# Kernel tuning notes

Hardware: AMD Instinct MI355X
Metric: run time of the kernel (lower is better)

The kernel has to match this reference:

```python
import jax, jax.numpy as jnp
import numpy as np

DIM = 1024          # config.dim
HID = 1024          # config.expert_hidden, already multiple of 64
N_EXP = 8           # num_routed_experts
TOP_K = 2           # top_k_experts
N_LOOPS = 4         # recursive_loops
B, S = 4, 1024


def setup_inputs() -> dict:
    key = jax.random.key(0)
    ks = jax.random.split(key, 10)
    def init(k, shape, fan_in):
        return jax.random.normal(k, shape, jnp.float32) * (fan_in ** -0.5)
    return {
        "x": jax.random.normal(ks[0], (B, S, DIM), jnp.float32),
        # shared expert (stored as [in, out] so forward is x @ W)
        "sg": init(ks[1], (DIM, HID), DIM),
        "su": init(ks[2], (DIM, HID), DIM),
        "sd": init(ks[3], (HID, DIM), HID),
        # routed experts stacked: [E, in, out]
        "Wg": init(ks[4], (N_EXP, DIM, HID), DIM),
        "Wu": init(ks[5], (N_EXP, DIM, HID), DIM),
        "Wd": init(ks[6], (N_EXP, HID, DIM), HID),
        # router: Linear(2*dim -> E, bias=False), stored [2*dim, E]
        "Wr": init(ks[7], (2 * DIM, N_EXP), 2 * DIM),
        # loop embedding table [num_loops, dim]
        "loop_table": jax.random.normal(ks[8], (N_LOOPS, DIM), jnp.float32),
        "loop_idx": 1,
    }


def _swiglu(x, wg, wu, wd):
    return (jax.nn.silu(x @ wg) * (x @ wu)) @ wd


def reference(x, sg, su, sd, Wg, Wu, Wd, Wr, loop_table, loop_idx):
    b, s, d = x.shape
    n = b * s
    xf = x.reshape(n, d)

    # shared expert (always active)
    shared = _swiglu(xf, sg, su, sd)  # [n, d]

    # loop-aware router: concat(x, loop_emb) @ Wr
    loop_emb = loop_table[loop_idx]                               # [d]
    router_in = jnp.concatenate(
        [xf, jnp.broadcast_to(loop_emb, (n, d))], axis=-1)        # [n, 2d]
    logits = router_in @ Wr                                       # [n, E]
    probs = jax.nn.sigmoid(logits)
    topw, topi = jax.lax.top_k(probs, TOP_K)                      # [n, k]

    # combine weights: combine[n, e] = sum_k topw[n,k] * (topi[n,k]==e)
    combine = jnp.zeros((n, N_EXP), x.dtype).at[
        jnp.arange(n)[:, None], topi].add(topw)                   # [n, E]

    # per-expert SwiGLU, combined with routing weights.
    # (dense-over-experts formulation; math identical to sort/dispatch/scatter)
    gate = jnp.einsum('nd,edh->neh', xf, Wg)                      # [n, E, H]
    up = jnp.einsum('nd,edh->neh', xf, Wu)                        # [n, E, H]
    h = jax.nn.silu(gate) * up                                    # [n, E, H]
    routed = jnp.einsum('neh,ehd,ne->nd', h, Wd, combine)         # [n, d]

    return (shared + routed).reshape(b, s, d)
```

## Files before the change

### kernel.cpp

```cpp
#include <hip/hip_runtime.h>
#include <cstdint>
#include <cstddef>

typedef __attribute__((ext_vector_type(8))) short short8;
typedef __attribute__((ext_vector_type(4))) float floatx4;

#define NTOK   4096
#define NSLOT  12288
#define SHSLOT 8192
#define MAT_ELEMS (1024 * 1024)

__device__ __forceinline__ unsigned short f2b(float f) {
  unsigned u = __float_as_uint(f);
  u = (u + 0x7fffu + ((u >> 16) & 1u)) >> 16;
  return (unsigned short)u;
}
__device__ __forceinline__ float b2f(unsigned short b) {
  return __uint_as_float((unsigned)b << 16);
}

#define GLD16(gsrc, ldst)                                                              \
  __builtin_amdgcn_global_load_lds(                                                    \
      (const __attribute__((address_space(1))) unsigned int*)(gsrc),                   \
      (__attribute__((address_space(3))) unsigned int*)(ldst), 16, 0, 0)

#define T2PITCH 260

__global__ __launch_bounds__(256) void prep_kernel(
    const float* __restrict__ x, const float* __restrict__ Wr,
    const float* __restrict__ loopTable, const int* __restrict__ loopIdx,
    const float* __restrict__ Wg, const float* __restrict__ Wu,
    const float* __restrict__ Wd, const float* __restrict__ sg,
    const float* __restrict__ su, const float* __restrict__ sd,
    unsigned short* __restrict__ Xb, int* __restrict__ cnt,
    int* __restrict__ permSparse, float* __restrict__ wSparse,
    int2* __restrict__ tokenEPos, unsigned short* __restrict__ Wt) {
  __shared__ __align__(16) char shraw[128 * T2PITCH];
  float (*red)[16][8] = (float(*)[16][8])shraw;
  float (*sbias)[8] = (float(*)[8])(shraw + 2048);
  int* lcnt = (int*)(shraw + 2048 + 128);
  int* lbase = (int*)(shraw + 2048 + 160);

  int tid = threadIdx.x;
  int bid = blockIdx.x;

  if (bid >= 256) {
    int tt = bid - 256;
    int m = tt >> 6;
    int tl = tt & 63;
    int k0 = (tl >> 3) << 7;
    int n0 = (tl & 7) << 7;
    int type = m / 9, e = m % 9;
    const float* src;
    if (type == 0)      src = (e < 8) ? Wg + (size_t)e * MAT_ELEMS : sg;
    else if (type == 1) src = (e < 8) ? Wu + (size_t)e * MAT_ELEMS : su;
    else                src = (e < 8) ? Wd + (size_t)e * MAT_ELEMS : sd;

    int rsub = tid >> 5;
    int nl4 = (tid & 31) << 2;
    const float* srcb = src + (size_t)k0 * 1024 + n0;
#pragma unroll
    for (int j = 0; j < 16; ++j) {
      int r = (j << 3) + rsub;
      float4 v = *(const float4*)(srcb + (size_t)r * 1024 + nl4);
      char* p0 = shraw + (size_t)(nl4 + 0) * T2PITCH + (r << 1);
      *(unsigned short*)(p0)               = f2b(v.x);
      *(unsigned short*)(p0 + T2PITCH)     = f2b(v.y);
      *(unsigned short*)(p0 + 2 * T2PITCH) = f2b(v.z);
      *(unsigned short*)(p0 + 3 * T2PITCH) = f2b(v.w);
    }
    __syncthreads();

    int nrow = tid >> 4;
    int l16 = tid & 15;
    unsigned short* dstm = Wt + (size_t)m * MAT_ELEMS;
#pragma unroll
    for (int p = 0; p < 8; ++p) {
      int n = (p << 4) + nrow;
      const char* rb = shraw + (size_t)n * T2PITCH + (l16 << 4);
      uint4 o;
      o.x = *(const unsigned*)(rb + 0);
      o.y = *(const unsigned*)(rb + 4);
      o.z = *(const unsigned*)(rb + 8);
      o.w = *(const unsigned*)(rb + 12);
      *(uint4*)&dstm[(size_t)(n0 + n) * 1024 + k0 + (l16 << 3)] = o;
    }
    return;
  }

  int lane = tid & 63;
  int seg = __builtin_amdgcn_readfirstlane(tid >> 6);
  int tok0 = bid << 4;
  int t16 = lane >> 2;
  int part = lane & 3;
  int tok = tok0 + t16;

  if (tid < 8) lcnt[tid] = 0;

  float bp[8] = {0, 0, 0, 0, 0, 0, 0, 0};
  {
    const float* emb = loopTable + (size_t)(*loopIdx) * 1024;
    int d = seg * 256 + lane * 4;
    float4 ev = *(const float4*)(emb + d);
    float es[4] = {ev.x, ev.y, ev.z, ev.w};
#pragma unroll
    for (int r = 0; r < 4; r++) {
      const float4* w4 = (const float4*)(Wr + (size_t)(1024 + d + r) * 8);
      float4 wa = w4[0], wb = w4[1];
      float e1 = es[r];
      bp[0] += e1 * wa.x; bp[1] += e1 * wa.y; bp[2] += e1 * wa.z; bp[3] += e1 * wa.w;
      bp[4] += e1 * wb.x; bp[5] += e1 * wb.y; bp[6] += e1 * wb.z; bp[7] += e1 * wb.w;
    }
  }
#pragma unroll
  for (int off = 32; off > 0; off >>= 1)
#pragma unroll
    for (int e = 0; e < 8; e++) bp[e] += __shfl_xor(bp[e], off, 64);
  if (lane == 0)
#pragma unroll
    for (int e = 0; e < 8; e++) sbias[seg][e] = bp[e];

  float lg[8] = {0, 0, 0, 0, 0, 0, 0, 0};
  const float* xr = x + (size_t)tok * 1024 + seg * 256 + part * 64;
  const float* wrb = Wr + (size_t)(seg * 256 + part * 64) * 8;
  for (int i = 0; i < 64; i += 4) {
    float4 xv = *(const float4*)(xr + i);
    float xs[4] = {xv.x, xv.y, xv.z, xv.w};
#pragma unroll
    for (int r = 0; r < 4; r++) {
      const float4* w4 = (const float4*)(wrb + (size_t)(i + r) * 8);
      float4 wa = w4[0], wb = w4[1];
      float xv1 = xs[r];
      lg[0] += xv1 * wa.x; lg[1] += xv1 * wa.y; lg[2] += xv1 * wa.z; lg[3] += xv1 * wa.w;
      lg[4] += xv1 * wb.x; lg[5] += xv1 * wb.y; lg[6] += xv1 * wb.z; lg[7] += xv1 * wb.w;
    }
  }
#pragma unroll
  for (int off = 1; off < 4; off <<= 1)
#pragma unroll
    for (int e = 0; e < 8; e++) lg[e] += __shfl_xor(lg[e], off, 64);
  if (part == 0)
#pragma unroll
    for (int e = 0; e < 8; e++) red[seg][t16][e] = lg[e];
  __syncthreads();

  int i0s = 0, i1s = 0, pos0s = 0, pos1s = 0;
  float p0s = 0.f, p1s = 0.f;
  if (tid < 16) {
    float l[8];
#pragma unroll
    for (int e = 0; e < 8; e++)
      l[e] = red[0][tid][e] + red[1][tid][e] + red[2][tid][e] + red[3][tid][e] +
             sbias[0][e] + sbias[1][e] + sbias[2][e] + sbias[3][e];
    int i0 = 0; float l0 = l[0];
#pragma unroll
    for (int e = 1; e < 8; e++) if (l[e] > l0) { l0 = l[e]; i0 = e; }
    int i1 = -1; float l1 = -1e30f;
#pragma unroll
    for (int e = 0; e < 8; e++) if (e != i0 && l[e] > l1) { l1 = l[e]; i1 = e; }
    i0s = i0; i1s = i1;
    p0s = 1.0f / (1.0f + __expf(-l0));
    p1s = 1.0f / (1.0f + __expf(-l1));
    pos0s = atomicAdd(&lcnt[i0], 1);
    pos1s = atomicAdd(&lcnt[i1], 1);
  }
  __syncthreads();
  if (tid < 8) lbase[tid] = atomicAdd(&cnt[tid], lcnt[tid]);
  __syncthreads();
  if (tid < 16) {
    int tk = tok0 + tid;
    int pos0 = lbase[i0s] + pos0s;
    int pos1 = lbase[i1s] + pos1s;
    permSparse[i0s * NTOK + pos0] = tk; wSparse[i0s * NTOK + pos0] = p0s;
    permSparse[i1s * NTOK + pos1] = tk; wSparse[i1s * NTOK + pos1] = p1s;
    tokenEPos[tk * 2 + 0] = make_int2(i0s, pos0);
    tokenEPos[tk * 2 + 1] = make_int2(i1s, pos1);
  }

  const float4* xs4 = (const float4*)(x + (size_t)tok0 * 1024);
  uint2* dst = (uint2*)(Xb + (size_t)tok0 * 1024);
  for (int i = tid; i < 16 * 256; i += 256) {
    float4 v = xs4[i];
    uint2 pk;
    pk.x = (unsigned)f2b(v.x) | ((unsigned)f2b(v.y) << 16);
    pk.y = (unsigned)f2b(v.z) | ((unsigned)f2b(v.w) << 16);
    dst[i] = pk;
  }
}

__device__ __forceinline__ void expert_range(const int* __restrict__ cnt, int e,
                                             int& c, int& off) {
  if (e == 8) { c = NTOK; off = SHSLOT; return; }
  off = 0; c = 0;
#pragma unroll
  for (int i = 0; i < 8; i++) {
    int cv = cnt[i];
    if (i < e) off += cv;
    if (i == e) c = cv;
  }
}

__global__ __launch_bounds__(256, 2) void gateup_gemm(
    const unsigned short* __restrict__ Xb, const unsigned short* __restrict__ Wt,
    const int* __restrict__ cnt, const int* __restrict__ permSparse,
    const float* __restrict__ wSparse, unsigned short* __restrict__ Hbuf) {
  int e = blockIdx.z;
  int c, off;
  expert_range(cnt, e, c, off);
  int m0 = blockIdx.y << 7;
  if (m0 >= c) return;
  int row_base = off + m0;
  int valid_m = c - m0; if (valid_m > 128) valid_m = 128;
  int n0 = blockIdx.x << 7;

  __shared__ unsigned short sA[128 * 64];
  __shared__ unsigned short sG[128 * 64];
  __shared__ unsigned short sU[128 * 64];

  int tid = threadIdx.x;
  int wv = tid >> 6, lane = tid & 63;
  int wm = wv >> 1, wn = wv & 1;

  const unsigned short* Gg = Wt + (size_t)e * MAT_ELEMS + (size_t)n0 * 1024;
  const unsigned short* Ug = Wt + (size_t)(9 + e) * MAT_ELEMS + (size_t)n0 * 1024;

  int srow = lane >> 3, schunk = lane & 7;
  int swc = (schunk ^ srow) << 3;

  int myTok[4];
#pragma unroll
  for (int j = 0; j < 4; j++) {
    int r = m0 + (wv << 5) + (j << 3) + srow;
    if (e < 8) myTok[j] = (r < c) ? permSparse[e * NTOK + r] : 0;
    else       myTok[j] = (r < c) ? r : 0;
  }

  floatx4 accG[4][4], accU[4][4];
#pragma unroll
  for (int i = 0; i < 4; i++)
#pragma unroll
    for (int j = 0; j < 4; j++) {
      accG[i][j] = floatx4{0.f, 0.f, 0.f, 0.f};
      accU[i][j] = floatx4{0.f, 0.f, 0.f, 0.f};
    }

  for (int kk = 0; kk < 1024; kk += 64) {
    __syncthreads();
#pragma unroll
    for (int j = 0; j < 4; j++) {
      int rb = (wv << 5) + (j << 3);
      size_t gw = (size_t)(rb + srow) * 1024 + kk + swc;
      GLD16(Xb + (size_t)myTok[j] * 1024 + kk + swc, &sA[rb * 64]);
      GLD16(Gg + gw, &sG[rb * 64]);
      GLD16(Ug + gw, &sU[rb * 64]);
    }
    __syncthreads();
#pragma unroll
    for (int k0 = 0; k0 < 64; k0 += 32) {
      int swoff = (((lane >> 4) + (k0 >> 3)) ^ (lane & 7)) << 3;
      int arow = (wm << 6) + (lane & 15);
      short8 af[4];
#pragma unroll
      for (int mi = 0; mi < 4; mi++)
        af[mi] = *(const short8*)&sA[(arow + (mi << 4)) * 64 + swoff];
      int brow = (wn << 6) + (lane & 15);
#pragma unroll
      for (int ni = 0; ni < 4; ni++) {
        short8 gf = *(const short8*)&sG[(brow + (ni << 4)) * 64 + swoff];
        short8 uf = *(const short8*)&sU[(brow + (ni << 4)) * 64 + swoff];
#pragma unroll
        for (int mi = 0; mi < 4; mi++) {
          accG[mi][ni] = __builtin_amdgcn_mfma_f32_16x16x32_bf16(af[mi], gf, accG[mi][ni], 0, 0, 0);
          accU[mi][ni] = __builtin_amdgcn_mfma_f32_16x16x32_bf16(af[mi], uf, accU[mi][ni], 0, 0, 0);
        }
      }
    }
  }

  int colLane = lane & 15, quad = lane >> 4;
#pragma unroll
  for (int mi = 0; mi < 4; mi++) {
#pragma unroll
    for (int reg = 0; reg < 4; reg++) {
      int mrow = (wm << 6) + (mi << 4) + (quad << 2) + reg;
      if (mrow < valid_m) {
        int r = m0 + mrow;
        float w = (e < 8) ? wSparse[e * NTOK + r] : 1.0f;
        unsigned short* hr = Hbuf + (size_t)(row_base + mrow) * 1024 + n0 + (wn << 6) + colLane;
#pragma unroll
        for (int ni = 0; ni < 4; ni++) {
          float g = accG[mi][ni][reg];
          float u = accU[mi][ni][reg];
          float h = (g / (1.0f + __expf(-g))) * u * w;
          hr[ni << 4] = f2b(h);
        }
      }
    }
  }
}

__global__ __launch_bounds__(256, 2) void down_gemm(
    const unsigned short* __restrict__ Hbuf, const unsigned short* __restrict__ Wt,
    const int* __restrict__ cnt, unsigned short* __restrict__ Dbuf) {
  int e = blockIdx.z;
  int c, off;
  expert_range(cnt, e, c, off);
  int m0 = blockIdx.y << 7;
  if (m0 >= c) return;
  int row_base = off + m0;
  int valid_m = c - m0; if (valid_m > 128) valid_m = 128;
  int n0 = blockIdx.x << 7;

  __shared__ unsigned short sA[128 * 64];
  __shared__ unsigned short sB[128 * 64];

  int tid = threadIdx.x;
  int wv = tid >> 6, lane = tid & 63;
  int wm = wv >> 1, wn = wv & 1;

  const unsigned short* Ag = Hbuf + (size_t)row_base * 1024;
  const unsigned short* Bg = Wt + (size_t)(18 + e) * MAT_ELEMS + (size_t)n0 * 1024;

  int srow = lane >> 3, schunk = lane & 7;
  int swc = (schunk ^ srow) << 3;

  floatx4 acc[4][4];
#pragma unroll
  for (int i = 0; i < 4; i++)
#pragma unroll
    for (int j = 0; j < 4; j++) acc[i][j] = floatx4{0.f, 0.f, 0.f, 0.f};

  for (int kk = 0; kk < 1024; kk += 64) {
    __syncthreads();
#pragma unroll
    for (int j = 0; j < 4; j++) {
      int rb = (wv << 5) + (j << 3);
      size_t gw = (size_t)(rb + srow) * 1024 + kk + swc;
      GLD16(Ag + gw, &sA[rb * 64]);
      GLD16(Bg + gw, &sB[rb * 64]);
    }
    __syncthreads();
#pragma unroll
    for (int k0 = 0; k0 < 64; k0 += 32) {
      int swoff = (((lane >> 4) + (k0 >> 3)) ^ (lane & 7)) << 3;
      int arow = (wm << 6) + (lane & 15);
      short8 af[4];
#pragma unroll
      for (int mi = 0; mi < 4; mi++)
        af[mi] = *(const short8*)&sA[(arow + (mi << 4)) * 64 + swoff];
      int brow = (wn << 6) + (lane & 15);
#pragma unroll
      for (int ni = 0; ni < 4; ni++) {
        short8 bf = *(const short8*)&sB[(brow + (ni << 4)) * 64 + swoff];
#pragma unroll
        for (int mi = 0; mi < 4; mi++)
          acc[mi][ni] = __builtin_amdgcn_mfma_f32_16x16x32_bf16(af[mi], bf, acc[mi][ni], 0, 0, 0);
      }
    }
  }

  int colLane = lane & 15, quad = lane >> 4;
#pragma unroll
  for (int mi = 0; mi < 4; mi++) {
#pragma unroll
    for (int reg = 0; reg < 4; reg++) {
      int mrow = (wm << 6) + (mi << 4) + (quad << 2) + reg;
      if (mrow < valid_m) {
        unsigned short* dr = Dbuf + (size_t)(row_base + mrow) * 1024 + n0 + (wn << 6) + colLane;
#pragma unroll
        for (int ni = 0; ni < 4; ni++)
          dr[ni << 4] = f2b(acc[mi][ni][reg]);
      }
    }
  }
}

__global__ __launch_bounds__(256) void combine_kernel(
    const unsigned short* __restrict__ Dbuf, const int* __restrict__ cnt,
    const int2* __restrict__ tokenEPos, float* __restrict__ out) {
  __shared__ int soffs[8];
  if (threadIdx.x == 0) {
    int s = 0;
    for (int i = 0; i < 8; i++) { soffs[i] = s; s += cnt[i]; }
  }
  __syncthreads();
  int tok = (blockIdx.x << 1) + (threadIdx.x >> 7);
  int lane = threadIdx.x & 127;
  int2 a = tokenEPos[tok * 2 + 0];
  int2 b = tokenEPos[tok * 2 + 1];
  int s0 = soffs[a.x] + a.y;
  int s1 = soffs[b.x] + b.y;
  int ssh = SHSLOT + tok;
  int d = lane << 3;
  uint4 r0 = *(const uint4*)(Dbuf + (size_t)ssh * 1024 + d);
  uint4 r1 = *(const uint4*)(Dbuf + (size_t)s0 * 1024 + d);
  uint4 r2 = *(const uint4*)(Dbuf + (size_t)s1 * 1024 + d);
  float o[8];
  const unsigned* u0 = (const unsigned*)&r0;
  const unsigned* u1 = (const unsigned*)&r1;
  const unsigned* u2 = (const unsigned*)&r2;
#pragma unroll
  for (int i = 0; i < 4; i++) {
    o[2 * i + 0] = b2f((unsigned short)(u0[i] & 0xffff)) +
                   b2f((unsigned short)(u1[i] & 0xffff)) +
                   b2f((unsigned short)(u2[i] & 0xffff));
    o[2 * i + 1] = b2f((unsigned short)(u0[i] >> 16)) +
                   b2f((unsigned short)(u1[i] >> 16)) +
                   b2f((unsigned short)(u2[i] >> 16));
  }
  float* orow = out + (size_t)tok * 1024 + d;
  *(float4*)(orow + 0) = make_float4(o[0], o[1], o[2], o[3]);
  *(float4*)(orow + 4) = make_float4(o[4], o[5], o[6], o[7]);
}

extern "C" void kernel_launch(void* const* d_in, const int* in_sizes, int n_in,
                              void* d_out, int out_size, void* d_ws, size_t ws_size,
                              hipStream_t stream) {
  const float* x  = (const float*)d_in[0];
  const float* sg = (const float*)d_in[1];
  const float* su = (const float*)d_in[2];
  const float* sd = (const float*)d_in[3];
  const float* Wg = (const float*)d_in[4];
  const float* Wu = (const float*)d_in[5];
  const float* Wd = (const float*)d_in[6];
  const float* Wr = (const float*)d_in[7];
  const float* loopTable = (const float*)d_in[8];
  const int*   loopIdx   = (const int*)d_in[9];
  float* out = (float*)d_out;

  char* w = (char*)d_ws;
  unsigned short* Wt = (unsigned short*)w;    w += (size_t)27 * MAT_ELEMS * 2;
  unsigned short* Xb = (unsigned short*)w;    w += (size_t)NTOK * 1024 * 2;
  unsigned short* Hbuf = (unsigned short*)w;  w += (size_t)NSLOT * 1024 * 2;
  unsigned short* Dbuf = (unsigned short*)w;  w += (size_t)NSLOT * 1024 * 2;
  int*   cnt        = (int*)w;   w += 16 * 4;
  int*   permSparse = (int*)w;   w += (size_t)8 * NTOK * 4;
  float* wSparse    = (float*)w; w += (size_t)8 * NTOK * 4;
  int2*  tokenEPos  = (int2*)w;  w += (size_t)NTOK * 2 * 8;

  hipMemsetAsync(cnt, 0, 32, stream);
  prep_kernel<<<256 + 27 * 64, 256, 0, stream>>>(
      x, Wr, loopTable, loopIdx, Wg, Wu, Wd, sg, su, sd,
      Xb, cnt, permSparse, wSparse, tokenEPos, Wt);
  gateup_gemm<<<dim3(8, 32, 9), 256, 0, stream>>>(Xb, Wt, cnt, permSparse,
                                                  wSparse, Hbuf);
  down_gemm<<<dim3(8, 32, 9), 256, 0, stream>>>(Hbuf, Wt, cnt, Dbuf);
  combine_kernel<<<2048, 256, 0, stream>>>(Dbuf, cnt, tokenEPos, out);
}
```

Before: 294.3 us.

## Triple-buffer LDS k-tiles with async global-to-LDS loads in expert GEMMs

Replaces the single-buffered 64-wide k-loop in the gate/up and down GEMMs with a three-stage ring of 32-wide k-tiles. Loads for tile h+2 are issued before computing tile h, with explicit vmcnt waits and raw barriers, so global-to-LDS transfers overlap the MFMA work. The LDS layout is re-swizzled for the 32-wide tiles, and s_setprio raises wave priority around the MFMA block. LDS use grows, to 72KB per block for gate/up, which may limit the two-blocks-per-CU occupancy target, and the hand-counted vmcnt values must match the exact number of loads issued.

Result: slower. 304.9 us (+3.6%).

```diff
diff --git a/kernel.cpp b/kernel.cpp
--- a/kernel.cpp
+++ b/kernel.cpp
@@ -23,6 +23,8 @@
   __builtin_amdgcn_global_load_lds(                                                    \
       (const __attribute__((address_space(1))) unsigned int*)(gsrc),                   \
       (__attribute__((address_space(3))) unsigned int*)(ldst), 16, 0, 0)
+
+#define WAITVM(N) asm volatile("s_waitcnt vmcnt(" #N ")" ::: "memory")
 
 #define T2PITCH 260
 
@@ -213,9 +215,7 @@
   int valid_m = c - m0; if (valid_m > 128) valid_m = 128;
   int n0 = blockIdx.x << 7;
 
-  __shared__ unsigned short sA[128 * 64];
-  __shared__ unsigned short sG[128 * 64];
-  __shared__ unsigned short sU[128 * 64];
+  __shared__ __align__(16) char lds[3 * 24576];
 
   int tid = threadIdx.x;
   int wv = tid >> 6, lane = tid & 63;
@@ -224,15 +224,32 @@
   const unsigned short* Gg = Wt + (size_t)e * MAT_ELEMS + (size_t)n0 * 1024;
   const unsigned short* Ug = Wt + (size_t)(9 + e) * MAT_ELEMS + (size_t)n0 * 1024;
 
-  int srow = lane >> 3, schunk = lane & 7;
-  int swc = (schunk ^ srow) << 3;
-
-  int myTok[4];
-#pragma unroll
-  for (int j = 0; j < 4; j++) {
-    int r = m0 + (wv << 5) + (j << 3) + srow;
-    if (e < 8) myTok[j] = (r < c) ? permSparse[e * NTOK + r] : 0;
-    else       myTok[j] = (r < c) ? r : 0;
+  int g = lane >> 3, s8 = lane & 7, v = s8 ^ g;
+  int vr = v >> 2;
+  int c8 = (v & 3) << 3;
+  int rl[2]; rl[0] = (wv << 5) + (g << 1) + vr; rl[1] = rl[0] + 16;
+
+  const unsigned short* gA[2];
+#pragma unroll
+  for (int i = 0; i < 2; ++i) {
+    int r = m0 + rl[i];
+    int tok;
+    if (e < 8) tok = (r < c) ? permSparse[e * NTOK + r] : 0;
+    else       tok = (r < c) ? r : 0;
+    gA[i] = Xb + (size_t)tok * 1024;
+  }
+  const unsigned short* gG[2] = { Gg + (size_t)rl[0] * 1024, Gg + (size_t)rl[1] * 1024 };
+  const unsigned short* gU[2] = { Ug + (size_t)rl[0] * 1024, Ug + (size_t)rl[1] * 1024 };
+  int ib[2] = { (wv << 11), (wv << 11) + 1024 };
+
+  int q = lane >> 4;
+  int offA[4], offB[4];
+#pragma unroll
+  for (int i = 0; i < 4; ++i) {
+    int rA = (wm << 6) + (lane & 15) + (i << 4);
+    offA[i] = ((rA >> 1) << 7) + (((((rA & 1) << 2) + q) ^ ((rA >> 1) & 7)) << 4);
+    int rB = (wn << 6) + (lane & 15) + (i << 4);
+    offB[i] = ((rB >> 1) << 7) + (((((rB & 1) << 2) + q) ^ ((rB >> 1) & 7)) << 4);
   }
 
   floatx4 accG[4][4], accU[4][4];
@@ -244,38 +261,46 @@
       accU[i][j] = floatx4{0.f, 0.f, 0.f, 0.f};
     }
 
-  for (int kk = 0; kk < 1024; kk += 64) {
-    __syncthreads();
-#pragma unroll
-    for (int j = 0; j < 4; j++) {
-      int rb = (wv << 5) + (j << 3);
-      size_t gw = (size_t)(rb + srow) * 1024 + kk + swc;
-      GLD16(Xb + (size_t)myTok[j] * 1024 + kk + swc, &sA[rb * 64]);
-      GLD16(Gg + gw, &sG[rb * 64]);
-      GLD16(Ug + gw, &sU[rb * 64]);
-    }
-    __syncthreads();
-#pragma unroll
-    for (int k0 = 0; k0 < 64; k0 += 32) {
-      int swoff = (((lane >> 4) + (k0 >> 3)) ^ (lane & 7)) << 3;
-      int arow = (wm << 6) + (lane & 15);
-      short8 af[4];
-#pragma unroll
-      for (int mi = 0; mi < 4; mi++)
-        af[mi] = *(const short8*)&sA[(arow + (mi << 4)) * 64 + swoff];
-      int brow = (wn << 6) + (lane & 15);
-#pragma unroll
-      for (int ni = 0; ni < 4; ni++) {
-        short8 gf = *(const short8*)&sG[(brow + (ni << 4)) * 64 + swoff];
-        short8 uf = *(const short8*)&sU[(brow + (ni << 4)) * 64 + swoff];
-#pragma unroll
-        for (int mi = 0; mi < 4; mi++) {
-          accG[mi][ni] = __builtin_amdgcn_mfma_f32_16x16x32_bf16(af[mi], gf, accG[mi][ni], 0, 0, 0);
-          accU[mi][ni] = __builtin_amdgcn_mfma_f32_16x16x32_bf16(af[mi], uf, accU[mi][ni], 0, 0, 0);
-        }
+#define GU_STAGE(SB, H) do { int ke = ((H) << 5) + c8;                     \
+    GLD16(gA[0] + ke, lds + (SB) + ib[0]);                                 \
+    GLD16(gA[1] + ke, lds + (SB) + ib[1]);                                 \
+    GLD16(gG[0] + ke, lds + (SB) + 8192 + ib[0]);                          \
+    GLD16(gG[1] + ke, lds + (SB) + 8192 + ib[1]);                          \
+    GLD16(gU[0] + ke, lds + (SB) + 16384 + ib[0]);                         \
+    GLD16(gU[1] + ke, lds + (SB) + 16384 + ib[1]); } while (0)
+
+  int sb0 = 0, sb1 = 24576, sb2 = 49152;
+  GU_STAGE(sb0, 0);
+  GU_STAGE(sb1, 1);
+
+  for (int h = 0; h < 32; ++h) {
+    __builtin_amdgcn_s_barrier();
+    __builtin_amdgcn_sched_barrier(0);
+    if (h < 30) GU_STAGE(sb2, h + 2);
+    if (h < 30)       WAITVM(12);
+    else if (h == 30) WAITVM(6);
+    else              WAITVM(0);
+    __builtin_amdgcn_s_barrier();
+    __builtin_amdgcn_sched_barrier(0);
+    short8 af[4];
+#pragma unroll
+    for (int mi = 0; mi < 4; ++mi)
+      af[mi] = *(const short8*)(lds + sb0 + offA[mi]);
+    __builtin_amdgcn_s_setprio(1);
+#pragma unroll
+    for (int ni = 0; ni < 4; ++ni) {
+      short8 gf = *(const short8*)(lds + sb0 + 8192 + offB[ni]);
+      short8 uf = *(const short8*)(lds + sb0 + 16384 + offB[ni]);
+#pragma unroll
+      for (int mi = 0; mi < 4; ++mi) {
+        accG[mi][ni] = __builtin_amdgcn_mfma_f32_16x16x32_bf16(af[mi], gf, accG[mi][ni], 0, 0, 0);
+        accU[mi][ni] = __builtin_amdgcn_mfma_f32_16x16x32_bf16(af[mi], uf, accU[mi][ni], 0, 0, 0);
       }
     }
-  }
+    __builtin_amdgcn_s_setprio(0);
+    int t = sb0; sb0 = sb1; sb1 = sb2; sb2 = t;
+  }
+#undef GU_STAGE
 
   int colLane = lane & 15, quad = lane >> 4;
 #pragma unroll
@@ -289,10 +314,10 @@
         unsigned short* hr = Hbuf + (size_t)(row_base + mrow) * 1024 + n0 + (wn << 6) + colLane;
 #pragma unroll
         for (int ni = 0; ni < 4; ni++) {
-          float g = accG[mi][ni][reg];
+          float gg2 = accG[mi][ni][reg];
           float u = accU[mi][ni][reg];
-          float h = (g / (1.0f + __expf(-g))) * u * w;
-          hr[ni << 4] = f2b(h);
+          float hh = (gg2 / (1.0f + __expf(-gg2))) * u * w;
+          hr[ni << 4] = f2b(hh);
         }
       }
     }
@@ -311,8 +336,7 @@
   int valid_m = c - m0; if (valid_m > 128) valid_m = 128;
   int n0 = blockIdx.x << 7;
 
-  __shared__ unsigned short sA[128 * 64];
-  __shared__ unsigned short sB[128 * 64];
+  __shared__ __align__(16) char lds[3 * 16384];
 
   int tid = threadIdx.x;
   int wv = tid >> 6, lane = tid & 63;
@@ -321,8 +345,24 @@
   const unsigned short* Ag = Hbuf + (size_t)row_base * 1024;
   const unsigned short* Bg = Wt + (size_t)(18 + e) * MAT_ELEMS + (size_t)n0 * 1024;
 
-  int srow = lane >> 3, schunk = lane & 7;
-  int swc = (schunk ^ srow) << 3;
+  int g = lane >> 3, s8 = lane & 7, v = s8 ^ g;
+  int vr = v >> 2;
+  int c8 = (v & 3) << 3;
+  int rl[2]; rl[0] = (wv << 5) + (g << 1) + vr; rl[1] = rl[0] + 16;
+
+  const unsigned short* gA[2] = { Ag + (size_t)rl[0] * 1024, Ag + (size_t)rl[1] * 1024 };
+  const unsigned short* gB[2] = { Bg + (size_t)rl[0] * 1024, Bg + (size_t)rl[1] * 1024 };
+  int ib[2] = { (wv << 11), (wv << 11) + 1024 };
+
+  int q = lane >> 4;
+  int offA[4], offB[4];
+#pragma unroll
+  for (int i = 0; i < 4; ++i) {
+    int rA = (wm << 6) + (lane & 15) + (i << 4);
+    offA[i] = ((rA >> 1) << 7) + (((((rA & 1) << 2) + q) ^ ((rA >> 1) & 7)) << 4);
+    int rB = (wn << 6) + (lane & 15) + (i << 4);
+    offB[i] = ((rB >> 1) << 7) + (((((rB & 1) << 2) + q) ^ ((rB >> 1) & 7)) << 4);
+  }
 
   floatx4 acc[4][4];
 #pragma unroll
@@ -330,34 +370,41 @@
 #pragma unroll
     for (int j = 0; j < 4; j++) acc[i][j] = floatx4{0.f, 0.f, 0.f, 0.f};
 
-  for (int kk = 0; kk < 1024; kk += 64) {
-    __syncthreads();
-#pragma unroll
-    for (int j = 0; j < 4; j++) {
-      int rb = (wv << 5) + (j << 3);
-      size_t gw = (size_t)(rb + srow) * 1024 + kk + swc;
-      GLD16(Ag + gw, &sA[rb * 64]);
-      GLD16(Bg + gw, &sB[rb * 64]);
-    }
-    __syncthreads();
-#pragma unroll
-    for (int k0 = 0; k0 < 64; k0 += 32) {
-      int swoff = (((lane >> 4) + (k0 >> 3)) ^ (lane & 7)) << 3;
-      int arow = (wm << 6) + (lane & 15);
-      short8 af[4];
-#pragma unroll
-      for (int mi = 0; mi < 4; mi++)
-        af[mi] = *(const short8*)&sA[(arow + (mi << 4)) * 64 + swoff];
-      int brow = (wn << 6) + (lane & 15);
-#pragma unroll
-      for (int ni = 0; ni < 4; ni++) {
-        short8 bf = *(const short8*)&sB[(brow + (ni << 4)) * 64 + swoff];
-#pragma unroll
-        for (int mi = 0; mi < 4; mi++)
-          acc[mi][ni] = __builtin_amdgcn_mfma_f32_16x16x32_bf16(af[mi], bf, acc[mi][ni], 0, 0, 0);
-      }
-    }
-  }
+#define DN_STAGE(SB, H) do { int ke = ((H) << 5) + c8;                     \
+    GLD16(gA[0] + ke, lds + (SB) + ib[0]);                                 \
+    GLD16(gA[1] + ke, lds + (SB) + ib[1]);                                 \
+    GLD16(gB[0] + ke, lds + (SB) + 8192 + ib[0]);                          \
+    GLD16(gB[1] + ke, lds + (SB) + 8192 + ib[1]); } while (0)
+
+  int sb0 = 0, sb1 = 16384, sb2 = 32768;
+  DN_STAGE(sb0, 0);
+  DN_STAGE(sb1, 1);
+
+  for (int h = 0; h < 32; ++h) {
+    __builtin_amdgcn_s_barrier();
+    __builtin_amdgcn_sched_barrier(0);
+    if (h < 30) DN_STAGE(sb2, h + 2);
+    if (h < 30)       WAITVM(8);
+    else if (h == 30) WAITVM(4);
+    else              WAITVM(0);
+    __builtin_amdgcn_s_barrier();
+    __builtin_amdgcn_sched_barrier(0);
+    short8 af[4];
+#pragma unroll
+    for (int mi = 0; mi < 4; ++mi)
+      af[mi] = *(const short8*)(lds + sb0 + offA[mi]);
+    __builtin_amdgcn_s_setprio(1);
+#pragma unroll
+    for (int ni = 0; ni < 4; ++ni) {
+      short8 bf = *(const short8*)(lds + sb0 + 8192 + offB[ni]);
+#pragma unroll
+      for (int mi = 0; mi < 4; ++mi)
+        acc[mi][ni] = __builtin_amdgcn_mfma_f32_16x16x32_bf16(af[mi], bf, acc[mi][ni], 0, 0, 0);
+    }
+    __builtin_amdgcn_s_setprio(0);
+    int t = sb0; sb0 = sb1; sb1 = sb2; sb2 = t;
+  }
+#undef DN_STAGE
 
   int colLane = lane & 15, quad = lane >> 4;
 #pragma unroll
```
